# Kernel optimization log

Measured on AMD Instinct MI355X. Metric: run time of the kernel, lower is better.

Reference implementation:

```python
import jax, jax.numpy as jnp
import numpy as np

B, S, D_IN, D_OUT = 1, 2048, 4096, 4096
N_HEADS, N_KV = 32, 8
HEAD_DIM = D_OUT // N_HEADS  # 128
GROUP = N_HEADS // N_KV      # 4


def _rope_tables(seq_len, head_dim, base=10000.0):
    inv = 1.0 / (base ** (np.arange(0, head_dim, 2, dtype=np.float32) / head_dim))
    t = np.arange(seq_len, dtype=np.float32)
    ang = np.outer(t, inv)                       # [S, hd/2]
    ang = np.concatenate([ang, ang], axis=-1)    # [S, hd]
    return jnp.asarray(np.cos(ang)), jnp.asarray(np.sin(ang))


def setup_inputs() -> dict:
    key = jax.random.key(0)
    kx, kq, kk, kv, ko = jax.random.split(key, 5)
    cos, sin = _rope_tables(S, HEAD_DIM)
    sc = 0.02
    return {
        "x": jax.random.normal(kx, (B, S, D_IN), dtype=jnp.float32),
        "cos": cos,
        "sin": sin,
        "Wq": jax.random.normal(kq, (D_OUT, D_IN), dtype=jnp.float32) * sc,
        "Wk": jax.random.normal(kk, (N_KV * HEAD_DIM, D_IN), dtype=jnp.float32) * sc,
        "Wv": jax.random.normal(kv, (N_KV * HEAD_DIM, D_IN), dtype=jnp.float32) * sc,
        "Wo": jax.random.normal(ko, (D_OUT, D_OUT), dtype=jnp.float32) * sc,
    }


def _apply_rope(t, cos, sin):
    # t: [b, h, s, hd]; cos/sin: [s, hd] -> rotate-half RoPE
    hd = t.shape[-1]
    x1, x2 = t[..., : hd // 2], t[..., hd // 2 :]
    rotated = jnp.concatenate([-x2, x1], axis=-1)
    return t * cos[None, None] + rotated * sin[None, None]


def reference(x, cos, sin, Wq, Wk, Wv, Wo):
    b, s, _ = x.shape
    q = (x @ Wq.T).reshape(b, s, N_HEADS, HEAD_DIM).transpose(0, 2, 1, 3)  # [b,H,s,hd]
    k = (x @ Wk.T).reshape(b, s, N_KV, HEAD_DIM).transpose(0, 2, 1, 3)     # [b,G,s,hd]
    v = (x @ Wv.T).reshape(b, s, N_KV, HEAD_DIM).transpose(0, 2, 1, 3)
    q = _apply_rope(q, cos, sin)
    k = _apply_rope(k, cos, sin)
    k = jnp.repeat(k, GROUP, axis=1)  # [b,H,s,hd]
    v = jnp.repeat(v, GROUP, axis=1)
    scores = jnp.einsum("bhqd,bhkd->bhqk", q, k)
    causal = jnp.triu(jnp.ones((s, s), dtype=bool), k=1)
    scores = jnp.where(causal[None, None], -jnp.inf, scores)
    attn = jax.nn.softmax(scores / jnp.sqrt(jnp.float32(HEAD_DIM)), axis=-1)
    ctx = jnp.einsum("bhqk,bhkd->bhqd", attn, v)
    ctx = ctx.transpose(0, 2, 1, 3).reshape(b, s, D_OUT)
    return ctx @ Wo.T
```

## Files before the change

kernel.cpp:

```cpp
#include <hip/hip_runtime.h>


typedef __bf16 bf16;
typedef __bf16 bf16x4 __attribute__((ext_vector_type(4)));
typedef __bf16 bf16x8 __attribute__((ext_vector_type(8)));
typedef float  f32x4  __attribute__((ext_vector_type(4)));

#define S_LEN   2048
#define DMODEL  4096
#define QKV_N   6144
#define K_OFF   4096
#define V_OFF   5120
#define HD      128
#define ATT_SCALE 0.08838834764831845f

__device__ __forceinline__ void gload16(const bf16* g, bf16* l) {
    __builtin_amdgcn_global_load_lds(
        (__attribute__((address_space(1))) void*)(g),
        (__attribute__((address_space(3))) void*)(l),
        16, 0, 0);
}

__global__ __launch_bounds__(256) void cast_f32_bf16(const float* __restrict__ in,
                                                     bf16* __restrict__ out, int n4) {
    int i = blockIdx.x * 256 + threadIdx.x;
    if (i >= n4) return;
    float4 v = reinterpret_cast<const float4*>(in)[i];
    bf16x4 o;
    o[0] = (bf16)v.x; o[1] = (bf16)v.y; o[2] = (bf16)v.z; o[3] = (bf16)v.w;
    reinterpret_cast<bf16x4*>(out)[i] = o;
}

template <typename OutT>
__global__ __launch_bounds__(256) void gemm_bt(const bf16* __restrict__ A,
                                               const bf16* __restrict__ B,
                                               OutT* __restrict__ C,
                                               int M, int N, int K, int ldc) {
    __shared__ bf16 As[128 * 32];
    __shared__ bf16 Bs[128 * 32];
    const int t    = threadIdx.x;
    const int wave = t >> 6, lane = t & 63;
    const int quad = lane >> 4, l15 = lane & 15;
    const int wm = (wave >> 1) * 64, wn = (wave & 1) * 64;
    const int bm = blockIdx.y * 128, bn = blockIdx.x * 128;

    f32x4 acc[4][4];
#pragma unroll
    for (int i = 0; i < 4; ++i)
#pragma unroll
        for (int j = 0; j < 4; ++j) acc[i][j] = (f32x4){0.f, 0.f, 0.f, 0.f};

    const int soff  = t * 8;
    const int arow0 = soff >> 5;
    const int acol  = soff & 31;

    for (int k0 = 0; k0 < K; k0 += 32) {
        __syncthreads();
#pragma unroll
        for (int it = 0; it < 2; ++it) {
            gload16(A + (size_t)(bm + arow0 + it * 64) * K + k0 + acol,
                    As + it * 2048 + wave * 512);
            gload16(B + (size_t)(bn + arow0 + it * 64) * K + k0 + acol,
                    Bs + it * 2048 + wave * 512);
        }
        __syncthreads();

        bf16x8 af[4], bfb[4];
#pragma unroll
        for (int i = 0; i < 4; ++i)
            af[i] = *reinterpret_cast<const bf16x8*>(&As[(wm + i * 16 + l15) * 32 + quad * 8]);
#pragma unroll
        for (int j = 0; j < 4; ++j)
            bfb[j] = *reinterpret_cast<const bf16x8*>(&Bs[(wn + j * 16 + l15) * 32 + quad * 8]);
#pragma unroll
        for (int i = 0; i < 4; ++i)
#pragma unroll
            for (int j = 0; j < 4; ++j)
                acc[i][j] = __builtin_amdgcn_mfma_f32_16x16x32_bf16(af[i], bfb[j], acc[i][j], 0, 0, 0);
    }

#pragma unroll
    for (int i = 0; i < 4; ++i) {
        const int m0 = bm + wm + i * 16 + quad * 4;
#pragma unroll
        for (int j = 0; j < 4; ++j) {
            const int n = bn + wn + j * 16 + l15;
#pragma unroll
            for (int r = 0; r < 4; ++r)
                C[(size_t)(m0 + r) * ldc + n] = (OutT)acc[i][j][r];
        }
    }
}

__global__ __launch_bounds__(256) void rope_kernel(bf16* __restrict__ qkv,
                                                   const float* __restrict__ cosT,
                                                   const float* __restrict__ sinT) {
    const int col = blockIdx.x * 256 + threadIdx.x;
    if (col >= 40 * 64) return;
    const int row  = blockIdx.y;
    const int head = col >> 6, d = col & 63;
    const size_t base = (size_t)row * QKV_N + head * 128 + d;
    const float x1 = (float)qkv[base];
    const float x2 = (float)qkv[base + 64];
    const float c  = cosT[row * 128 + d];
    const float s  = sinT[row * 128 + d];
    qkv[base]      = (bf16)(x1 * c - x2 * s);
    qkv[base + 64] = (bf16)(x2 * c + x1 * s);
}

__global__ __launch_bounds__(256) void transpose_v(const bf16* __restrict__ qkv,
                                                   bf16* __restrict__ vt) {
    __shared__ bf16 T[64][72];
    const int c0 = blockIdx.x * 64;
    const int s0 = blockIdx.y * 64;
    const int t  = threadIdx.x;
#pragma unroll
    for (int it = 0; it < 2; ++it) {
        const int sl = (t >> 3) + it * 32;
        const int c8 = (t & 7) * 8;
        bf16x8 v = *reinterpret_cast<const bf16x8*>(
            qkv + (size_t)(s0 + sl) * QKV_N + V_OFF + c0 + c8);
        *reinterpret_cast<bf16x8*>(&T[sl][c8]) = v;
    }
    __syncthreads();
#pragma unroll
    for (int it = 0; it < 2; ++it) {
        const int cl = (t >> 3) + it * 32;
        const int s8 = (t & 7) * 8;
        bf16x8 o;
#pragma unroll
        for (int e = 0; e < 8; ++e) o[e] = T[s8 + e][cl];
        *reinterpret_cast<bf16x8*>(vt + (size_t)(c0 + cl) * S_LEN + s0 + s8) = o;
    }
}

__global__ __launch_bounds__(512) void flash_attn(const bf16* __restrict__ qkv,
                                                  const bf16* __restrict__ vt,
                                                  bf16* __restrict__ ctx) {
    const int blk   = blockIdx.x;
    const int qtile = 15 - (blk >> 5);
    const int h     = blk & 31;
    const int kh    = h >> 2;
    const int q0    = qtile * 128;
    const int t     = threadIdx.x;
    const int wave  = t >> 6, lane = t & 63;
    const int quad  = lane >> 4, l15 = lane & 15;

    __shared__ bf16 Ks[64 * 128];
    __shared__ bf16 Vs[128 * 64];
    __shared__ bf16 Ps[8 * 16 * 72];

    const bf16* Qb  = qkv + h * HD;
    const bf16* Kb  = qkv + K_OFF + kh * HD;
    const bf16* Vth = vt + (size_t)kh * HD * S_LEN;

    const int qrow_a = q0 + wave * 16 + l15;
    bf16x8 qf[4];
#pragma unroll
    for (int kk = 0; kk < 4; ++kk)
        qf[kk] = *reinterpret_cast<const bf16x8*>(
            Qb + (size_t)qrow_a * QKV_N + kk * 32 + quad * 8);

    float m_i[4], l_i[4];
    f32x4 o_acc[8];
#pragma unroll
    for (int r = 0; r < 4; ++r) { m_i[r] = -1e30f; l_i[r] = 0.f; }
#pragma unroll
    for (int dt = 0; dt < 8; ++dt) o_acc[dt] = (f32x4){0.f, 0.f, 0.f, 0.f};

    const int myrow = q0 + wave * 16 + quad * 4;
    bf16* PsW = Ps + wave * (16 * 72);

    for (int kv0 = 0; kv0 < q0 + 128; kv0 += 64) {
        __syncthreads();
#pragma unroll
        for (int it = 0; it < 2; ++it) {
            const int rb = wave * 8 + it * 4;
            const int r  = rb + (lane >> 4);
            const int cg = (lane & 15) ^ (r & 15);
            gload16(Kb + (size_t)(kv0 + r) * QKV_N + cg * 8, Ks + rb * 128);
        }
#pragma unroll
        for (int it = 0; it < 2; ++it) {
            const int db = wave * 16 + it * 8;
            const int d  = db + (lane >> 3);
            const int cg = (lane & 7) ^ (d & 7);
            gload16(Vth + (size_t)d * S_LEN + kv0 + cg * 8, Vs + db * 64);
        }
        __syncthreads();

        float sv[4][4];
        const bool need_mask = (kv0 + 63) > q0;
#pragma unroll
        for (int j = 0; j < 4; ++j) {
            f32x4 s = (f32x4){0.f, 0.f, 0.f, 0.f};
#pragma unroll
            for (int kk = 0; kk < 4; ++kk) {
                const int cd = kk * 4 + quad;
                bf16x8 kf = *reinterpret_cast<const bf16x8*>(
                    &Ks[(j * 16 + l15) * 128 + ((cd ^ l15) & 15) * 8]);
                s = __builtin_amdgcn_mfma_f32_16x16x32_bf16(qf[kk], kf, s, 0, 0, 0);
            }
            if (need_mask) {
#pragma unroll
                for (int r = 0; r < 4; ++r)
                    sv[j][r] = ((kv0 + j * 16 + l15) <= (myrow + r))
                                   ? s[r] * ATT_SCALE : -1e30f;
            } else {
#pragma unroll
                for (int r = 0; r < 4; ++r) sv[j][r] = s[r] * ATT_SCALE;
            }
        }

        float al[4];
#pragma unroll
        for (int r = 0; r < 4; ++r) {
            float mt = fmaxf(fmaxf(sv[0][r], sv[1][r]), fmaxf(sv[2][r], sv[3][r]));
#pragma unroll
            for (int off = 1; off < 16; off <<= 1) mt = fmaxf(mt, __shfl_xor(mt, off));
            const float mn = fmaxf(m_i[r], mt);
            al[r] = __expf(m_i[r] - mn);
            m_i[r] = mn;
            float rs = 0.f;
#pragma unroll
            for (int j = 0; j < 4; ++j) {
                const float p = __expf(sv[j][r] - mn);
                rs += p;
                PsW[(quad * 4 + r) * 72 + j * 16 + l15] = (bf16)p;
            }
#pragma unroll
            for (int off = 1; off < 16; off <<= 1) rs += __shfl_xor(rs, off);
            l_i[r] = l_i[r] * al[r] + rs;
        }

#pragma unroll
        for (int dt = 0; dt < 8; ++dt) {
            o_acc[dt][0] *= al[0]; o_acc[dt][1] *= al[1];
            o_acc[dt][2] *= al[2]; o_acc[dt][3] *= al[3];
        }

        bf16x8 pa[2];
        pa[0] = *reinterpret_cast<const bf16x8*>(&PsW[l15 * 72 + quad * 8]);
        pa[1] = *reinterpret_cast<const bf16x8*>(&PsW[l15 * 72 + 32 + quad * 8]);
#pragma unroll
        for (int dt = 0; dt < 8; ++dt) {
#pragma unroll
            for (int c = 0; c < 2; ++c) {
                const int ck = c * 4 + quad;
                bf16x8 vb = *reinterpret_cast<const bf16x8*>(
                    &Vs[(dt * 16 + l15) * 64 + ((ck ^ (l15 & 7)) & 7) * 8]);
                o_acc[dt] = __builtin_amdgcn_mfma_f32_16x16x32_bf16(pa[c], vb, o_acc[dt], 0, 0, 0);
            }
        }
    }

#pragma unroll
    for (int dt = 0; dt < 8; ++dt)
#pragma unroll
        for (int r = 0; r < 4; ++r)
            ctx[(size_t)(myrow + r) * DMODEL + h * HD + dt * 16 + l15] =
                (bf16)(o_acc[dt][r] / l_i[r]);
}

extern "C" void kernel_launch(void* const* d_in, const int* in_sizes, int n_in,
                              void* d_out, int out_size, void* d_ws, size_t ws_size,
                              hipStream_t stream) {
    const float* x    = (const float*)d_in[0];
    const float* cosT = (const float*)d_in[1];
    const float* sinT = (const float*)d_in[2];
    const float* Wq   = (const float*)d_in[3];
    const float* Wk   = (const float*)d_in[4];
    const float* Wv   = (const float*)d_in[5];
    const float* Wo   = (const float*)d_in[6];
    float* out = (float*)d_out;

    bf16* xb   = (bf16*)d_ws;
    bf16* Wqkv = xb   + (size_t)S_LEN * DMODEL;
    bf16* Wob  = Wqkv + (size_t)QKV_N * DMODEL;
    bf16* QKV  = Wob  + (size_t)DMODEL * DMODEL;
    bf16* ctx  = QKV  + (size_t)S_LEN * QKV_N;
    bf16* Vt   = ctx  + (size_t)S_LEN * DMODEL;

    cast_f32_bf16<<<(S_LEN * DMODEL / 4 + 255) / 256, 256, 0, stream>>>(x, xb, S_LEN * DMODEL / 4);
    cast_f32_bf16<<<(DMODEL * DMODEL / 4 + 255) / 256, 256, 0, stream>>>(Wq, Wqkv, DMODEL * DMODEL / 4);
    cast_f32_bf16<<<(1024 * DMODEL / 4 + 255) / 256, 256, 0, stream>>>(
        Wk, Wqkv + (size_t)4096 * DMODEL, 1024 * DMODEL / 4);
    cast_f32_bf16<<<(1024 * DMODEL / 4 + 255) / 256, 256, 0, stream>>>(
        Wv, Wqkv + (size_t)5120 * DMODEL, 1024 * DMODEL / 4);
    cast_f32_bf16<<<(DMODEL * DMODEL / 4 + 255) / 256, 256, 0, stream>>>(Wo, Wob, DMODEL * DMODEL / 4);

    gemm_bt<bf16><<<dim3(QKV_N / 128, S_LEN / 128), 256, 0, stream>>>(
        xb, Wqkv, QKV, S_LEN, QKV_N, DMODEL, QKV_N);

    rope_kernel<<<dim3(10, S_LEN), 256, 0, stream>>>(QKV, cosT, sinT);

    transpose_v<<<dim3(16, 32), 256, 0, stream>>>(QKV, Vt);

    flash_attn<<<dim3(16 * 32), 512, 0, stream>>>(QKV, Vt, ctx);

    gemm_bt<float><<<dim3(DMODEL / 128, S_LEN / 128), 256, 0, stream>>>(
        ctx, Wob, out, S_LEN, DMODEL, DMODEL, DMODEL);
}
```

Baseline: 558.9 us.

## Swizzle GEMM LDS, vectorize RoPE, restructure flash attention to direct loads

The GEMM LDS tile gets an XOR swizzle on both the async global-to-LDS stores and the fragment reads, to cut bank conflicts. RoPE is rewritten so each thread handles 8 elements with 16-byte vector loads and stores, one block per row. Flash attention drops LDS staging of K/V: 4 waves each own 32 query rows (two 16-row groups) and read K and V^T fragments straight from global memory, each wave stops at its own causal bound, and q-tiles are ordered to balance work. This removes block-wide barriers and shared K/V traffic, but relies on cache hits for the now-redundant per-wave global loads.

After: 630.6 us. +12.8%, slower.

```diff
diff --git a/kernel.cpp b/kernel.cpp
--- a/kernel.cpp
+++ b/kernel.cpp
@@ -50,28 +50,31 @@
 #pragma unroll
         for (int j = 0; j < 4; ++j) acc[i][j] = (f32x4){0.f, 0.f, 0.f, 0.f};
 
-    const int soff  = t * 8;
-    const int arow0 = soff >> 5;
-    const int acol  = soff & 31;
+    const int srow = t >> 2;
+    const int scol = ((t & 3) ^ ((srow >> 1) & 3)) * 8;
 
     for (int k0 = 0; k0 < K; k0 += 32) {
         __syncthreads();
 #pragma unroll
         for (int it = 0; it < 2; ++it) {
-            gload16(A + (size_t)(bm + arow0 + it * 64) * K + k0 + acol,
+            gload16(A + (size_t)(bm + srow + it * 64) * K + k0 + scol,
                     As + it * 2048 + wave * 512);
-            gload16(B + (size_t)(bn + arow0 + it * 64) * K + k0 + acol,
+            gload16(B + (size_t)(bn + srow + it * 64) * K + k0 + scol,
                     Bs + it * 2048 + wave * 512);
         }
         __syncthreads();
 
         bf16x8 af[4], bfb[4];
 #pragma unroll
-        for (int i = 0; i < 4; ++i)
-            af[i] = *reinterpret_cast<const bf16x8*>(&As[(wm + i * 16 + l15) * 32 + quad * 8]);
-#pragma unroll
-        for (int j = 0; j < 4; ++j)
-            bfb[j] = *reinterpret_cast<const bf16x8*>(&Bs[(wn + j * 16 + l15) * 32 + quad * 8]);
+        for (int i = 0; i < 4; ++i) {
+            const int r = wm + i * 16 + l15;
+            af[i] = *reinterpret_cast<const bf16x8*>(&As[r * 32 + (quad ^ ((r >> 1) & 3)) * 8]);
+        }
+#pragma unroll
+        for (int j = 0; j < 4; ++j) {
+            const int r = wn + j * 16 + l15;
+            bfb[j] = *reinterpret_cast<const bf16x8*>(&Bs[r * 32 + (quad ^ ((r >> 1) & 3)) * 8]);
+        }
 #pragma unroll
         for (int i = 0; i < 4; ++i)
 #pragma unroll
@@ -92,20 +95,30 @@
     }
 }
 
-__global__ __launch_bounds__(256) void rope_kernel(bf16* __restrict__ qkv,
+__global__ __launch_bounds__(320) void rope_kernel(bf16* __restrict__ qkv,
                                                    const float* __restrict__ cosT,
                                                    const float* __restrict__ sinT) {
-    const int col = blockIdx.x * 256 + threadIdx.x;
-    if (col >= 40 * 64) return;
-    const int row  = blockIdx.y;
-    const int head = col >> 6, d = col & 63;
-    const size_t base = (size_t)row * QKV_N + head * 128 + d;
-    const float x1 = (float)qkv[base];
-    const float x2 = (float)qkv[base + 64];
-    const float c  = cosT[row * 128 + d];
-    const float s  = sinT[row * 128 + d];
-    qkv[base]      = (bf16)(x1 * c - x2 * s);
-    qkv[base + 64] = (bf16)(x2 * c + x1 * s);
+    const int u    = threadIdx.x;
+    const int row  = blockIdx.x;
+    const int head = u >> 3, d0 = (u & 7) * 8;
+    bf16* p = qkv + (size_t)row * QKV_N + head * 128 + d0;
+    bf16x8 a = *reinterpret_cast<const bf16x8*>(p);
+    bf16x8 b = *reinterpret_cast<const bf16x8*>(p + 64);
+    const float4 c0 = *reinterpret_cast<const float4*>(cosT + row * 128 + d0);
+    const float4 c1 = *reinterpret_cast<const float4*>(cosT + row * 128 + d0 + 4);
+    const float4 s0 = *reinterpret_cast<const float4*>(sinT + row * 128 + d0);
+    const float4 s1 = *reinterpret_cast<const float4*>(sinT + row * 128 + d0 + 4);
+    float c[8] = {c0.x, c0.y, c0.z, c0.w, c1.x, c1.y, c1.z, c1.w};
+    float s[8] = {s0.x, s0.y, s0.z, s0.w, s1.x, s1.y, s1.z, s1.w};
+    bf16x8 oa, ob;
+#pragma unroll
+    for (int e = 0; e < 8; ++e) {
+        const float x1 = (float)a[e], x2 = (float)b[e];
+        oa[e] = (bf16)(x1 * c[e] - x2 * s[e]);
+        ob[e] = (bf16)(x2 * c[e] + x1 * s[e]);
+    }
+    *reinterpret_cast<bf16x8*>(p)      = oa;
+    *reinterpret_cast<bf16x8*>(p + 64) = ob;
 }
 
 __global__ __launch_bounds__(256) void transpose_v(const bf16* __restrict__ qkv,
@@ -134,11 +147,12 @@
     }
 }
 
-__global__ __launch_bounds__(512) void flash_attn(const bf16* __restrict__ qkv,
-                                                  const bf16* __restrict__ vt,
-                                                  bf16* __restrict__ ctx) {
+__global__ __launch_bounds__(256, 2) void flash_attn(const bf16* __restrict__ qkv,
+                                                     const bf16* __restrict__ vt,
+                                                     bf16* __restrict__ ctx) {
     const int blk   = blockIdx.x;
-    const int qtile = 15 - (blk >> 5);
+    const int idx   = blk >> 5;
+    const int qtile = (idx < 8) ? (15 - idx) : (idx - 8);
     const int h     = blk & 31;
     const int kh    = h >> 2;
     const int q0    = qtile * 128;
@@ -146,120 +160,129 @@
     const int wave  = t >> 6, lane = t & 63;
     const int quad  = lane >> 4, l15 = lane & 15;
 
-    __shared__ bf16 Ks[64 * 128];
-    __shared__ bf16 Vs[128 * 64];
-    __shared__ bf16 Ps[8 * 16 * 72];
+    __shared__ bf16 Ps[4 * 2 * 16 * 72];
 
     const bf16* Qb  = qkv + h * HD;
     const bf16* Kb  = qkv + K_OFF + kh * HD;
     const bf16* Vth = vt + (size_t)kh * HD * S_LEN;
 
-    const int qrow_a = q0 + wave * 16 + l15;
-    bf16x8 qf[4];
-#pragma unroll
-    for (int kk = 0; kk < 4; ++kk)
-        qf[kk] = *reinterpret_cast<const bf16x8*>(
-            Qb + (size_t)qrow_a * QKV_N + kk * 32 + quad * 8);
-
-    float m_i[4], l_i[4];
-    f32x4 o_acc[8];
-#pragma unroll
-    for (int r = 0; r < 4; ++r) { m_i[r] = -1e30f; l_i[r] = 0.f; }
-#pragma unroll
-    for (int dt = 0; dt < 8; ++dt) o_acc[dt] = (f32x4){0.f, 0.f, 0.f, 0.f};
-
-    const int myrow = q0 + wave * 16 + quad * 4;
-    bf16* PsW = Ps + wave * (16 * 72);
-
-    for (int kv0 = 0; kv0 < q0 + 128; kv0 += 64) {
-        __syncthreads();
-#pragma unroll
-        for (int it = 0; it < 2; ++it) {
-            const int rb = wave * 8 + it * 4;
-            const int r  = rb + (lane >> 4);
-            const int cg = (lane & 15) ^ (r & 15);
-            gload16(Kb + (size_t)(kv0 + r) * QKV_N + cg * 8, Ks + rb * 128);
-        }
-#pragma unroll
-        for (int it = 0; it < 2; ++it) {
-            const int db = wave * 16 + it * 8;
-            const int d  = db + (lane >> 3);
-            const int cg = (lane & 7) ^ (d & 7);
-            gload16(Vth + (size_t)d * S_LEN + kv0 + cg * 8, Vs + db * 64);
-        }
-        __syncthreads();
-
-        float sv[4][4];
-        const bool need_mask = (kv0 + 63) > q0;
+    bf16x8 qf[2][4];
+#pragma unroll
+    for (int g = 0; g < 2; ++g) {
+        const int qrow = q0 + wave * 32 + g * 16 + l15;
+#pragma unroll
+        for (int kk = 0; kk < 4; ++kk)
+            qf[g][kk] = *reinterpret_cast<const bf16x8*>(
+                Qb + (size_t)qrow * QKV_N + kk * 32 + quad * 8);
+    }
+
+    float m_i[2][4], l_i[2][4];
+    f32x4 o_acc[2][8];
+#pragma unroll
+    for (int g = 0; g < 2; ++g) {
+#pragma unroll
+        for (int r = 0; r < 4; ++r) { m_i[g][r] = -1e30f; l_i[g][r] = 0.f; }
+#pragma unroll
+        for (int dt = 0; dt < 8; ++dt) o_acc[g][dt] = (f32x4){0.f, 0.f, 0.f, 0.f};
+    }
+
+    const int grow0 = q0 + wave * 32 + quad * 4;
+    bf16* PsW[2] = {Ps + (wave * 2 + 0) * (16 * 72), Ps + (wave * 2 + 1) * (16 * 72)};
+
+    const int kv_end = q0 + wave * 32 + 32;
+
+    for (int kv0 = 0; kv0 < kv_end; kv0 += 64) {
+        float sv[2][4][4];
+        const int gbase0 = q0 + wave * 32;
 #pragma unroll
         for (int j = 0; j < 4; ++j) {
-            f32x4 s = (f32x4){0.f, 0.f, 0.f, 0.f};
+            f32x4 s0 = (f32x4){0.f, 0.f, 0.f, 0.f};
+            f32x4 s1 = (f32x4){0.f, 0.f, 0.f, 0.f};
+            const bf16* krow = Kb + (size_t)(kv0 + j * 16 + l15) * QKV_N + quad * 8;
 #pragma unroll
             for (int kk = 0; kk < 4; ++kk) {
-                const int cd = kk * 4 + quad;
-                bf16x8 kf = *reinterpret_cast<const bf16x8*>(
-                    &Ks[(j * 16 + l15) * 128 + ((cd ^ l15) & 15) * 8]);
-                s = __builtin_amdgcn_mfma_f32_16x16x32_bf16(qf[kk], kf, s, 0, 0, 0);
-            }
-            if (need_mask) {
+                bf16x8 kf = *reinterpret_cast<const bf16x8*>(krow + kk * 32);
+                s0 = __builtin_amdgcn_mfma_f32_16x16x32_bf16(qf[0][kk], kf, s0, 0, 0, 0);
+                s1 = __builtin_amdgcn_mfma_f32_16x16x32_bf16(qf[1][kk], kf, s1, 0, 0, 0);
+            }
+            const int kvc = kv0 + j * 16 + l15;
+            if (kv0 + 63 > gbase0) {
 #pragma unroll
                 for (int r = 0; r < 4; ++r)
-                    sv[j][r] = ((kv0 + j * 16 + l15) <= (myrow + r))
-                                   ? s[r] * ATT_SCALE : -1e30f;
+                    sv[0][j][r] = (kvc <= grow0 + r) ? s0[r] * ATT_SCALE : -1e30f;
             } else {
 #pragma unroll
-                for (int r = 0; r < 4; ++r) sv[j][r] = s[r] * ATT_SCALE;
-            }
-        }
-
-        float al[4];
-#pragma unroll
-        for (int r = 0; r < 4; ++r) {
-            float mt = fmaxf(fmaxf(sv[0][r], sv[1][r]), fmaxf(sv[2][r], sv[3][r]));
-#pragma unroll
-            for (int off = 1; off < 16; off <<= 1) mt = fmaxf(mt, __shfl_xor(mt, off));
-            const float mn = fmaxf(m_i[r], mt);
-            al[r] = __expf(m_i[r] - mn);
-            m_i[r] = mn;
-            float rs = 0.f;
-#pragma unroll
-            for (int j = 0; j < 4; ++j) {
-                const float p = __expf(sv[j][r] - mn);
-                rs += p;
-                PsW[(quad * 4 + r) * 72 + j * 16 + l15] = (bf16)p;
-            }
-#pragma unroll
-            for (int off = 1; off < 16; off <<= 1) rs += __shfl_xor(rs, off);
-            l_i[r] = l_i[r] * al[r] + rs;
-        }
-
+                for (int r = 0; r < 4; ++r) sv[0][j][r] = s0[r] * ATT_SCALE;
+            }
+            if (kv0 + 63 > gbase0 + 16) {
+#pragma unroll
+                for (int r = 0; r < 4; ++r)
+                    sv[1][j][r] = (kvc <= grow0 + 16 + r) ? s1[r] * ATT_SCALE : -1e30f;
+            } else {
+#pragma unroll
+                for (int r = 0; r < 4; ++r) sv[1][j][r] = s1[r] * ATT_SCALE;
+            }
+        }
+
+        float al[2][4];
+#pragma unroll
+        for (int g = 0; g < 2; ++g) {
+#pragma unroll
+            for (int r = 0; r < 4; ++r) {
+                float mt = fmaxf(fmaxf(sv[g][0][r], sv[g][1][r]),
+                                 fmaxf(sv[g][2][r], sv[g][3][r]));
+#pragma unroll
+                for (int off = 1; off < 16; off <<= 1) mt = fmaxf(mt, __shfl_xor(mt, off));
+                const float mn = fmaxf(m_i[g][r], mt);
+                al[g][r] = __expf(m_i[g][r] - mn);
+                m_i[g][r] = mn;
+                float rs = 0.f;
+#pragma unroll
+                for (int j = 0; j < 4; ++j) {
+                    const float p = __expf(sv[g][j][r] - mn);
+                    rs += p;
+                    PsW[g][(quad * 4 + r) * 72 + j * 16 + l15] = (bf16)p;
+                }
+#pragma unroll
+                for (int off = 1; off < 16; off <<= 1) rs += __shfl_xor(rs, off);
+                l_i[g][r] = l_i[g][r] * al[g][r] + rs;
+            }
+        }
+
+#pragma unroll
+        for (int g = 0; g < 2; ++g)
+#pragma unroll
+            for (int dt = 0; dt < 8; ++dt) {
+                o_acc[g][dt][0] *= al[g][0]; o_acc[g][dt][1] *= al[g][1];
+                o_acc[g][dt][2] *= al[g][2]; o_acc[g][dt][3] *= al[g][3];
+            }
+
+        bf16x8 pa[2][2];
+#pragma unroll
+        for (int g = 0; g < 2; ++g) {
+            pa[g][0] = *reinterpret_cast<const bf16x8*>(&PsW[g][l15 * 72 + quad * 8]);
+            pa[g][1] = *reinterpret_cast<const bf16x8*>(&PsW[g][l15 * 72 + 32 + quad * 8]);
+        }
 #pragma unroll
         for (int dt = 0; dt < 8; ++dt) {
-            o_acc[dt][0] *= al[0]; o_acc[dt][1] *= al[1];
-            o_acc[dt][2] *= al[2]; o_acc[dt][3] *= al[3];
-        }
-
-        bf16x8 pa[2];
-        pa[0] = *reinterpret_cast<const bf16x8*>(&PsW[l15 * 72 + quad * 8]);
-        pa[1] = *reinterpret_cast<const bf16x8*>(&PsW[l15 * 72 + 32 + quad * 8]);
-#pragma unroll
-        for (int dt = 0; dt < 8; ++dt) {
+            const bf16* vrow = Vth + (size_t)(dt * 16 + l15) * S_LEN + kv0 + quad * 8;
 #pragma unroll
             for (int c = 0; c < 2; ++c) {
-                const int ck = c * 4 + quad;
-                bf16x8 vb = *reinterpret_cast<const bf16x8*>(
-                    &Vs[(dt * 16 + l15) * 64 + ((ck ^ (l15 & 7)) & 7) * 8]);
-                o_acc[dt] = __builtin_amdgcn_mfma_f32_16x16x32_bf16(pa[c], vb, o_acc[dt], 0, 0, 0);
-            }
-        }
-    }
-
-#pragma unroll
-    for (int dt = 0; dt < 8; ++dt)
-#pragma unroll
-        for (int r = 0; r < 4; ++r)
-            ctx[(size_t)(myrow + r) * DMODEL + h * HD + dt * 16 + l15] =
-                (bf16)(o_acc[dt][r] / l_i[r]);
+                bf16x8 vb = *reinterpret_cast<const bf16x8*>(vrow + c * 32);
+                o_acc[0][dt] = __builtin_amdgcn_mfma_f32_16x16x32_bf16(pa[0][c], vb, o_acc[0][dt], 0, 0, 0);
+                o_acc[1][dt] = __builtin_amdgcn_mfma_f32_16x16x32_bf16(pa[1][c], vb, o_acc[1][dt], 0, 0, 0);
+            }
+        }
+    }
+
+#pragma unroll
+    for (int g = 0; g < 2; ++g)
+#pragma unroll
+        for (int dt = 0; dt < 8; ++dt)
+#pragma unroll
+            for (int r = 0; r < 4; ++r)
+                ctx[(size_t)(grow0 + g * 16 + r) * DMODEL + h * HD + dt * 16 + l15] =
+                    (bf16)(o_acc[g][dt][r] / l_i[g][r]);
 }
 
 extern "C" void kernel_launch(void* const* d_in, const int* in_sizes, int n_in,
@@ -292,11 +315,11 @@
     gemm_bt<bf16><<<dim3(QKV_N / 128, S_LEN / 128), 256, 0, stream>>>(
         xb, Wqkv, QKV, S_LEN, QKV_N, DMODEL, QKV_N);
 
-    rope_kernel<<<dim3(10, S_LEN), 256, 0, stream>>>(QKV, cosT, sinT);
+    rope_kernel<<<dim3(S_LEN), 320, 0, stream>>>(QKV, cosT, sinT);
 
     transpose_v<<<dim3(16, 32), 256, 0, stream>>>(QKV, Vt);
 
-    flash_attn<<<dim3(16 * 32), 512, 0, stream>>>(QKV, Vt, ctx);
+    flash_attn<<<dim3(16 * 32), 256, 0, stream>>>(QKV, Vt, ctx);
 
     gemm_bt<float><<<dim3(DMODEL / 128, S_LEN / 128), 256, 0, stream>>>(
         ctx, Wob, out, S_LEN, DMODEL, DMODEL, DMODEL);
```
